# Kernel tuning notes

Hardware: AMD Instinct MI355X
Metric: run time of the kernel (lower is better)

Reference implementation:

```python
import jax, jax.numpy as jnp
import numpy as np

N = 20480    # total nodes in batched graph (64 graphs x 320 nodes)
E = 327680   # edges, avg in-degree 16
G = 64       # graphs in the batch
IN_DIM = 128
H = 4        # attention heads per layer
D = 64       # hidden dim per head (num_hidden)
C = 10       # num_classes
NEG_SLOPE = 0.2


def _gat_layer(h, src, dst, W, al, ar, residual):
    # DGL GATConv: fc -> per-head attention logits -> edge softmax over dst -> scatter-sum
    z = (h @ W).reshape(N, H, D)                       # [N,H,D]
    el = jnp.sum(z * al, axis=-1)                      # [N,H]
    er = jnp.sum(z * ar, axis=-1)                      # [N,H]
    e = jax.nn.leaky_relu(el[src] + er[dst], NEG_SLOPE)  # [E,H]
    m = jax.lax.stop_gradient(jax.ops.segment_max(e, dst, num_segments=N))
    m = jnp.where(jnp.isfinite(m), m, 0.0)
    ex = jnp.exp(e - m[dst])                           # [E,H]
    s = jax.ops.segment_sum(ex, dst, num_segments=N)   # [N,H]
    a = ex / jnp.where(s > 0, s, 1.0)[dst]             # [E,H] edge softmax
    msg = z[src] * a[:, :, None]                       # [E,H,D] (dominant intermediate)
    out = jax.ops.segment_sum(msg, dst, num_segments=N)  # [N,H,D]
    if residual:
        out = out + h.reshape(N, H, D)                 # res_fc is Identity (in == H*D)
        out = jax.nn.elu(out)                          # GATConv-internal activation
    return jax.nn.elu(out.reshape(N, H * D))           # model-level activation after flatten


def setup_inputs() -> dict:
    key = jax.random.key(0)
    ks = jax.random.split(key, 16)
    x = jax.random.normal(ks[0], (N, IN_DIM), jnp.float32)
    src = jax.random.randint(ks[1], (E,), 0, N, dtype=jnp.int32)
    # guarantee every node has >= 1 incoming edge (valid softmax denominator)
    dst = jnp.concatenate([jnp.arange(N, dtype=jnp.int32),
                           jax.random.randint(ks[2], (E - N,), 0, N, dtype=jnp.int32)])
    graph_ids = jnp.repeat(jnp.arange(G, dtype=jnp.int32), N // G)

    def lin(k, fi, fo):
        return (jax.random.normal(k, (fi, fo), jnp.float32) / np.float32(np.sqrt(fi)))

    def attn(k):
        return jax.random.normal(k, (H, D), jnp.float32) * np.float32(0.1)

    return {
        "x": x, "src": src, "dst": dst, "graph_ids": graph_ids,
        "W0": lin(ks[3], IN_DIM, H * D), "al0": attn(ks[4]), "ar0": attn(ks[5]),
        "W1": lin(ks[6], H * D, H * D), "al1": attn(ks[7]), "ar1": attn(ks[8]),
        "W2": lin(ks[9], H * D, H * D), "al2": attn(ks[10]), "ar2": attn(ks[11]),
        "Wc": lin(ks[12], H * D, C),
        "bc": jnp.zeros((C,), jnp.float32),
    }


def reference(x, src, dst, graph_ids, W0, al0, ar0, W1, al1, ar1, W2, al2, ar2, Wc, bc):
    h = _gat_layer(x, src, dst, W0, al0, ar0, residual=False)  # layer 0: no residual/act inside
    h = _gat_layer(h, src, dst, W1, al1, ar1, residual=True)
    h = _gat_layer(h, src, dst, W2, al2, ar2, residual=True)
    # dgl.mean_nodes: per-graph mean over node features
    hg = jax.ops.segment_sum(h, graph_ids, num_segments=G) / np.float32(N // G)  # [G, H*D]
    hg = jax.nn.elu(hg)
    return hg @ Wc + bc                                        # [G, C] logits
```

## Files before the change

kernel.cpp:

```cpp
#include <hip/hip_runtime.h>


#define NNODES 20480
#define NEDGES 327680
#define NGRAPH 64
#define NPG    320
#define HD     256
#define NH     4
#define NCLS   10
#define SLOTS  80

typedef __attribute__((ext_vector_type(8))) short short8;
typedef __attribute__((ext_vector_type(4))) float f32x4;

__device__ __forceinline__ float elu_f(float x)   { return x > 0.f ? x : expm1f(x); }
__device__ __forceinline__ float lrelu_f(float x) { return x > 0.f ? x : 0.2f * x; }

__device__ __forceinline__ ushort f2bf(float v) {
    uint u = __float_as_uint(v);
    uint r = (u + 0x7fffu + ((u >> 16) & 1u)) >> 16;
    return (ushort)r;
}
__device__ __forceinline__ float bf2f(ushort u) {
    return __uint_as_float(((uint)u) << 16);
}

__device__ __forceinline__ void split8(const float* __restrict__ p,
                                       short8& hi, short8& lo) {
    float4 a = *reinterpret_cast<const float4*>(p);
    float4 b = *reinterpret_cast<const float4*>(p + 4);
    float v[8] = {a.x, a.y, a.z, a.w, b.x, b.y, b.z, b.w};
    #pragma unroll
    for (int e = 0; e < 8; e++) {
        uint u = __float_as_uint(v[e]);
        hi[e] = (short)(u >> 16);
        float hf = __uint_as_float(u & 0xFFFF0000u);
        float lf = v[e] - hf;
        lo[e] = (short)(__float_as_uint(lf) >> 16);
    }
}

__global__ __launch_bounds__(256) void prep_k(
        const int* __restrict__ src, const int* __restrict__ dst,
        int* __restrict__ deg, int* __restrict__ slots,
        const float* __restrict__ W0, ushort* __restrict__ B0h, ushort* __restrict__ B0l,
        const float* __restrict__ W1, ushort* __restrict__ B1h, ushort* __restrict__ B1l,
        const float* __restrict__ W2, ushort* __restrict__ B2h, ushort* __restrict__ B2l) {
    int b = blockIdx.x;
    if (b < NEDGES / 256) {
        int e = b * 256 + threadIdx.x;
        int d = dst[e];
        int pos = atomicAdd(&deg[d], 1);
        if (pos < SLOTS) slots[d * SLOTS + pos] = src[e];
    } else {
        int idx = (b - NEDGES / 256) * 256 + threadIdx.x;
        const float* W; ushort *Bh, *Bl;
        if (idx < 128 * 256)          { W = W0; Bh = B0h; Bl = B0l; }
        else if (idx < 384 * 256)     { W = W1; Bh = B1h; Bl = B1l; idx -= 128 * 256; }
        else                          { W = W2; Bh = B2h; Bl = B2l; idx -= 384 * 256; }
        int k = idx >> 8, col = idx & 255;
        float v = W[idx];
        ushort h = f2bf(v);
        float vh = bf2f(h);
        ushort l = f2bf(v - vh);
        size_t o = (size_t)(k >> 5) * 8192 + (size_t)col * 32 + (k & 31);
        Bh[o] = h;
        Bl[o] = l;
    }
}

__global__ __launch_bounds__(256) void gemm_mfma_k(
        const float* __restrict__ A,
        const ushort* __restrict__ Bhi, const ushort* __restrict__ Blo,
        const float* __restrict__ al_, const float* __restrict__ ar_,
        ushort* __restrict__ zbf, float* __restrict__ el, float* __restrict__ er,
        int K) {
    int m0 = blockIdx.x * 32;
    int w = threadIdx.x >> 6, l = threadIdx.x & 63;
    int n0 = w * 64;
    int lr = l & 15, lk = l >> 4;
    f32x4 acc[2][4] = {};
    int ksteps = K >> 5;
    for (int kt = 0; kt < ksteps; kt++) {
        int kbase = kt * 32 + lk * 8;
        short8 a_hi[2], a_lo[2], b_hi[4], b_lo[4];
        #pragma unroll
        for (int i = 0; i < 2; i++) {
            size_t off = (size_t)(m0 + i * 16 + lr) * K + kbase;
            split8(A + off, a_hi[i], a_lo[i]);
        }
        #pragma unroll
        for (int j = 0; j < 4; j++) {
            size_t off = (size_t)kt * 8192 + (size_t)(n0 + j * 16 + lr) * 32 + lk * 8;
            b_hi[j] = *reinterpret_cast<const short8*>(Bhi + off);
            b_lo[j] = *reinterpret_cast<const short8*>(Blo + off);
        }
        #pragma unroll
        for (int i = 0; i < 2; i++)
            #pragma unroll
            for (int j = 0; j < 4; j++) {
                acc[i][j] = __builtin_amdgcn_mfma_f32_16x16x32_bf16(a_hi[i], b_hi[j], acc[i][j], 0, 0, 0);
                acc[i][j] = __builtin_amdgcn_mfma_f32_16x16x32_bf16(a_hi[i], b_lo[j], acc[i][j], 0, 0, 0);
                acc[i][j] = __builtin_amdgcn_mfma_f32_16x16x32_bf16(a_lo[i], b_hi[j], acc[i][j], 0, 0, 0);
            }
    }
    float alv[4], arv[4];
    #pragma unroll
    for (int j = 0; j < 4; j++) {
        int col = n0 + j * 16 + lr;
        alv[j] = al_[col];
        arv[j] = ar_[col];
    }
    #pragma unroll
    for (int i = 0; i < 2; i++) {
        #pragma unroll
        for (int r = 0; r < 4; r++) {
            float pel = 0.f, per = 0.f;
            #pragma unroll
            for (int j = 0; j < 4; j++) {
                float v = acc[i][j][r];
                pel += v * alv[j];
                per += v * arv[j];
                int row = m0 + i * 16 + lk * 4 + r;
                int col = n0 + j * 16 + lr;
                zbf[(size_t)row * HD + col] = f2bf(v);
            }
            #pragma unroll
            for (int off = 1; off < 16; off <<= 1) {
                pel += __shfl_xor(pel, off);
                per += __shfl_xor(per, off);
            }
            if (lr == 0) {
                int row = m0 + i * 16 + lk * 4 + r;
                el[row * NH + w] = pel;
                er[row * NH + w] = per;
            }
        }
    }
}

__global__ __launch_bounds__(256) void attn_aggr_k(
        const ushort* __restrict__ zbf,
        const float* __restrict__ el, const float* __restrict__ er,
        const int* __restrict__ deg, const int* __restrict__ slots,
        const float* __restrict__ hin, float* __restrict__ hout,
        int residual) {
    int wid = threadIdx.x >> 6, lane = threadIdx.x & 63;
    int n = blockIdx.x * 4 + wid;
    int h = lane >> 4, j16 = lane & 15;
    int hbase = lane & 48;
    int col = j16 * 4 + h * 64;
    int d = deg[n];
    if (d > SLOTS) d = SLOTS;
    const int* sl = slots + (size_t)n * SLOTS;
    float ern = er[n * NH + h];
    float4 acc = make_float4(0.f, 0.f, 0.f, 0.f);

    if (d <= 64) {
        float pv[4];
        int   sv[4];
        #pragma unroll
        for (int u = 0; u < 4; u++) {
            int k = u * 16 + j16;
            if (k < d) {
                sv[u] = sl[k];
                pv[u] = __expf(lrelu_f(el[sv[u] * NH + h] + ern));
            } else {
                sv[u] = 0;
                pv[u] = 0.f;
            }
        }
        float ssum = pv[0] + pv[1] + pv[2] + pv[3];
        #pragma unroll
        for (int off = 1; off < 16; off <<= 1) ssum += __shfl_xor(ssum, off);
        float rinv = 1.f / ssum;
        #pragma unroll
        for (int u = 0; u < 4; u++) pv[u] *= rinv;
        #pragma unroll
        for (int u = 0; u < 4; u++) {
            int kb = u * 16;
            if (kb + 16 <= d) {
                #pragma unroll
                for (int j = 0; j < 16; j++) {
                    float w = __shfl(pv[u], hbase + j);
                    int   s = __shfl(sv[u], hbase + j);
                    ushort4 zv = *reinterpret_cast<const ushort4*>(&zbf[(size_t)s * HD + col]);
                    acc.x += bf2f(zv.x) * w;
                    acc.y += bf2f(zv.y) * w;
                    acc.z += bf2f(zv.z) * w;
                    acc.w += bf2f(zv.w) * w;
                }
            } else if (kb < d) {
                int cnt = d - kb;
                for (int j = 0; j < cnt; j++) {
                    float w = __shfl(pv[u], hbase + j);
                    int   s = __shfl(sv[u], hbase + j);
                    ushort4 zv = *reinterpret_cast<const ushort4*>(&zbf[(size_t)s * HD + col]);
                    acc.x += bf2f(zv.x) * w;
                    acc.y += bf2f(zv.y) * w;
                    acc.z += bf2f(zv.z) * w;
                    acc.w += bf2f(zv.w) * w;
                }
            }
        }
    } else {
        float ssum = 0.f;
        for (int k = j16; k < d; k += 16)
            ssum += __expf(lrelu_f(el[sl[k] * NH + h] + ern));
        #pragma unroll
        for (int off = 1; off < 16; off <<= 1) ssum += __shfl_xor(ssum, off);
        float rinv = 1.f / ssum;
        for (int k = 0; k < d; k++) {
            int s = sl[k];
            float w = __expf(lrelu_f(el[s * NH + h] + ern)) * rinv;
            ushort4 zv = *reinterpret_cast<const ushort4*>(&zbf[(size_t)s * HD + col]);
            acc.x += bf2f(zv.x) * w;
            acc.y += bf2f(zv.y) * w;
            acc.z += bf2f(zv.z) * w;
            acc.w += bf2f(zv.w) * w;
        }
    }

    size_t o = (size_t)n * HD + col;
    float4 r;
    if (residual) {
        float4 hv = *reinterpret_cast<const float4*>(&hin[o]);
        r.x = elu_f(elu_f(acc.x + hv.x));
        r.y = elu_f(elu_f(acc.y + hv.y));
        r.z = elu_f(elu_f(acc.z + hv.z));
        r.w = elu_f(elu_f(acc.w + hv.w));
    } else {
        r.x = elu_f(acc.x);
        r.y = elu_f(acc.y);
        r.z = elu_f(acc.z);
        r.w = elu_f(acc.w);
    }
    *reinterpret_cast<float4*>(&hout[o]) = r;
}

__global__ __launch_bounds__(1024) void poolcls_k(const float* __restrict__ h,
                                                  const float* __restrict__ Wc,
                                                  const float* __restrict__ bc,
                                                  float* __restrict__ out) {
    __shared__ float part[4][HD];
    __shared__ float hv[HD];
    int g = blockIdx.x, t = threadIdx.x;
    int col = t & 255, q = t >> 8;
    const float* p = h + (size_t)g * NPG * HD + (size_t)q * (NPG / 4) * HD + col;
    float s = 0.f;
    for (int i = 0; i < NPG / 4; i++) s += p[(size_t)i * HD];
    part[q][col] = s;
    __syncthreads();
    if (t < HD) {
        float tot = part[0][t] + part[1][t] + part[2][t] + part[3][t];
        hv[t] = elu_f(tot * (1.0f / NPG));
    }
    __syncthreads();
    if (t < NCLS) {
        float acc = bc[t];
        for (int k = 0; k < HD; k++) acc += hv[k] * Wc[k * NCLS + t];
        out[g * NCLS + t] = acc;
    }
}

extern "C" void kernel_launch(void* const* d_in, const int* in_sizes, int n_in,
                              void* d_out, int out_size, void* d_ws, size_t ws_size,
                              hipStream_t stream) {
    const float* x   = (const float*)d_in[0];
    const int*   src = (const int*)d_in[1];
    const int*   dst = (const int*)d_in[2];
    const float* W0  = (const float*)d_in[4];
    const float* al0 = (const float*)d_in[5];
    const float* ar0 = (const float*)d_in[6];
    const float* W1  = (const float*)d_in[7];
    const float* al1 = (const float*)d_in[8];
    const float* ar1 = (const float*)d_in[9];
    const float* W2  = (const float*)d_in[10];
    const float* al2 = (const float*)d_in[11];
    const float* ar2 = (const float*)d_in[12];
    const float* Wc  = (const float*)d_in[13];
    const float* bc  = (const float*)d_in[14];
    float* out = (float*)d_out;

    char* ws = (char*)d_ws;
    size_t off = 0;
    auto alloc = [&](size_t bytes) -> void* {
        void* p = ws + off;
        off = (off + bytes + 255) & ~(size_t)255;
        return p;
    };
    float*  hbuf     = (float*)alloc((size_t)NNODES * HD * 4);
    ushort* zbf      = (ushort*)alloc((size_t)NNODES * HD * 2);
    float*  el       = (float*)alloc((size_t)NNODES * NH * 4);
    float*  er       = (float*)alloc((size_t)NNODES * NH * 4);
    int*    deg      = (int*)alloc((size_t)NNODES * 4);
    int*    slots    = (int*)alloc((size_t)NNODES * SLOTS * 4);
    ushort* B0h      = (ushort*)alloc((size_t)128 * 256 * 2);
    ushort* B0l      = (ushort*)alloc((size_t)128 * 256 * 2);
    ushort* B1h      = (ushort*)alloc((size_t)256 * 256 * 2);
    ushort* B1l      = (ushort*)alloc((size_t)256 * 256 * 2);
    ushort* B2h      = (ushort*)alloc((size_t)256 * 256 * 2);
    ushort* B2l      = (ushort*)alloc((size_t)256 * 256 * 2);

    hipMemsetAsync(deg, 0, (size_t)NNODES * 4, stream);
    prep_k<<<NEDGES / 256 + (128 + 256 + 256), 256, 0, stream>>>(
        src, dst, deg, slots,
        W0, B0h, B0l, W1, B1h, B1l, W2, B2h, B2l);

    auto layer = [&](const float* A, const ushort* Bh, const ushort* Bl,
                     const float* al_, const float* ar_,
                     const float* hin, float* hout, int K, int residual) {
        gemm_mfma_k<<<NNODES / 32, 256, 0, stream>>>(A, Bh, Bl, al_, ar_,
                                                     zbf, el, er, K);
        attn_aggr_k<<<NNODES / 4, 256, 0, stream>>>(zbf, el, er, deg, slots,
                                                    hin, hout, residual);
    };

    layer(x,    B0h, B0l, al0, ar0, nullptr, hbuf, 128, 0);
    layer(hbuf, B1h, B1l, al1, ar1, hbuf, hbuf, 256, 1);
    layer(hbuf, B2h, B2l, al2, ar2, hbuf, hbuf, 256, 1);

    poolcls_k<<<NGRAPH, 1024, 0, stream>>>(hbuf, Wc, bc, out);
}
```

Before: 280.9 us.

## Store hidden activations in bf16 and widen aggregation gathers to 16 bytes

```diff
diff --git a/kernel.cpp b/kernel.cpp
--- a/kernel.cpp
+++ b/kernel.cpp
@@ -11,6 +11,7 @@
 #define SLOTS  80
 
 typedef __attribute__((ext_vector_type(8))) short short8;
+typedef __attribute__((ext_vector_type(8))) unsigned short ushort8v;
 typedef __attribute__((ext_vector_type(4))) float f32x4;
 
 __device__ __forceinline__ float elu_f(float x)   { return x > 0.f ? x : expm1f(x); }
@@ -69,8 +70,9 @@
     }
 }
 
+template<int ABF16>
 __global__ __launch_bounds__(256) void gemm_mfma_k(
-        const float* __restrict__ A,
+        const void* __restrict__ Av,
         const ushort* __restrict__ Bhi, const ushort* __restrict__ Blo,
         const float* __restrict__ al_, const float* __restrict__ ar_,
         ushort* __restrict__ zbf, float* __restrict__ el, float* __restrict__ er,
@@ -87,7 +89,11 @@
         #pragma unroll
         for (int i = 0; i < 2; i++) {
             size_t off = (size_t)(m0 + i * 16 + lr) * K + kbase;
-            split8(A + off, a_hi[i], a_lo[i]);
+            if (ABF16) {
+                a_hi[i] = *reinterpret_cast<const short8*>((const ushort*)Av + off);
+            } else {
+                split8((const float*)Av + off, a_hi[i], a_lo[i]);
+            }
         }
         #pragma unroll
         for (int j = 0; j < 4; j++) {
@@ -101,7 +107,8 @@
             for (int j = 0; j < 4; j++) {
                 acc[i][j] = __builtin_amdgcn_mfma_f32_16x16x32_bf16(a_hi[i], b_hi[j], acc[i][j], 0, 0, 0);
                 acc[i][j] = __builtin_amdgcn_mfma_f32_16x16x32_bf16(a_hi[i], b_lo[j], acc[i][j], 0, 0, 0);
-                acc[i][j] = __builtin_amdgcn_mfma_f32_16x16x32_bf16(a_lo[i], b_hi[j], acc[i][j], 0, 0, 0);
+                if (!ABF16)
+                    acc[i][j] = __builtin_amdgcn_mfma_f32_16x16x32_bf16(a_lo[i], b_hi[j], acc[i][j], 0, 0, 0);
             }
     }
     float alv[4], arv[4];
@@ -143,18 +150,19 @@
         const ushort* __restrict__ zbf,
         const float* __restrict__ el, const float* __restrict__ er,
         const int* __restrict__ deg, const int* __restrict__ slots,
-        const float* __restrict__ hin, float* __restrict__ hout,
+        const ushort* __restrict__ hin, ushort* __restrict__ hout,
         int residual) {
     int wid = threadIdx.x >> 6, lane = threadIdx.x & 63;
     int n = blockIdx.x * 4 + wid;
     int h = lane >> 4, j16 = lane & 15;
-    int hbase = lane & 48;
-    int col = j16 * 4 + h * 64;
+    int l32 = lane & 31, half = lane >> 5;
+    int headL = l32 >> 3;
+    int col8 = l32 * 8;
     int d = deg[n];
     if (d > SLOTS) d = SLOTS;
     const int* sl = slots + (size_t)n * SLOTS;
     float ern = er[n * NH + h];
-    float4 acc = make_float4(0.f, 0.f, 0.f, 0.f);
+    float acc[8] = {};
 
     if (d <= 64) {
         float pv[4];
@@ -178,31 +186,22 @@
         for (int u = 0; u < 4; u++) pv[u] *= rinv;
         #pragma unroll
         for (int u = 0; u < 4; u++) {
-            int kb = u * 16;
-            if (kb + 16 <= d) {
-                #pragma unroll
-                for (int j = 0; j < 16; j++) {
-                    float w = __shfl(pv[u], hbase + j);
-                    int   s = __shfl(sv[u], hbase + j);
-                    ushort4 zv = *reinterpret_cast<const ushort4*>(&zbf[(size_t)s * HD + col]);
-                    acc.x += bf2f(zv.x) * w;
-                    acc.y += bf2f(zv.y) * w;
-                    acc.z += bf2f(zv.z) * w;
-                    acc.w += bf2f(zv.w) * w;
+            if (u * 16 >= d) break;
+            #pragma unroll
+            for (int jj = 0; jj < 8; jj++) {
+                int e = u * 16 + jj * 2 + half;
+                int srcl = headL * 16 + jj * 2 + half;
+                float w = __shfl(pv[u], srcl);
+                int   s = __shfl(sv[u], srcl);
+                if (e < d) {
+                    ushort8v zv = *reinterpret_cast<const ushort8v*>(&zbf[(size_t)s * HD + col8]);
+                    #pragma unroll
+                    for (int t = 0; t < 8; t++) acc[t] += bf2f(zv[t]) * w;
                 }
-            } else if (kb < d) {
-                int cnt = d - kb;
-                for (int j = 0; j < cnt; j++) {
-                    float w = __shfl(pv[u], hbase + j);
-                    int   s = __shfl(sv[u], hbase + j);
-                    ushort4 zv = *reinterpret_cast<const ushort4*>(&zbf[(size_t)s * HD + col]);
-                    acc.x += bf2f(zv.x) * w;
-                    acc.y += bf2f(zv.y) * w;
-                    acc.z += bf2f(zv.z) * w;
-                    acc.w += bf2f(zv.w) * w;
-                }
-            }
-        }
+            }
+        }
+        #pragma unroll
+        for (int t = 0; t < 8; t++) acc[t] += __shfl_xor(acc[t], 32);
     } else {
         float ssum = 0.f;
         for (int k = j16; k < d; k += 16)
@@ -210,35 +209,35 @@
         #pragma unroll
         for (int off = 1; off < 16; off <<= 1) ssum += __shfl_xor(ssum, off);
         float rinv = 1.f / ssum;
+        float rinvL = __shfl(rinv, headL * 16);
+        float ernL = er[n * NH + headL];
         for (int k = 0; k < d; k++) {
             int s = sl[k];
-            float w = __expf(lrelu_f(el[s * NH + h] + ern)) * rinv;
-            ushort4 zv = *reinterpret_cast<const ushort4*>(&zbf[(size_t)s * HD + col]);
-            acc.x += bf2f(zv.x) * w;
-            acc.y += bf2f(zv.y) * w;
-            acc.z += bf2f(zv.z) * w;
-            acc.w += bf2f(zv.w) * w;
-        }
-    }
-
-    size_t o = (size_t)n * HD + col;
-    float4 r;
-    if (residual) {
-        float4 hv = *reinterpret_cast<const float4*>(&hin[o]);
-        r.x = elu_f(elu_f(acc.x + hv.x));
-        r.y = elu_f(elu_f(acc.y + hv.y));
-        r.z = elu_f(elu_f(acc.z + hv.z));
-        r.w = elu_f(elu_f(acc.w + hv.w));
-    } else {
-        r.x = elu_f(acc.x);
-        r.y = elu_f(acc.y);
-        r.z = elu_f(acc.z);
-        r.w = elu_f(acc.w);
-    }
-    *reinterpret_cast<float4*>(&hout[o]) = r;
-}
-
-__global__ __launch_bounds__(1024) void poolcls_k(const float* __restrict__ h,
+            float w = __expf(lrelu_f(el[s * NH + headL] + ernL)) * rinvL;
+            ushort8v zv = *reinterpret_cast<const ushort8v*>(&zbf[(size_t)s * HD + col8]);
+            #pragma unroll
+            for (int t = 0; t < 8; t++) acc[t] += bf2f(zv[t]) * w;
+        }
+    }
+
+    if (half == 0) {
+        size_t o = (size_t)n * HD + col8;
+        ushort8v r;
+        if (residual) {
+            ushort8v hv = *reinterpret_cast<const ushort8v*>(&hin[o]);
+            #pragma unroll
+            for (int t = 0; t < 8; t++)
+                r[t] = f2bf(elu_f(elu_f(acc[t] + bf2f(hv[t]))));
+        } else {
+            #pragma unroll
+            for (int t = 0; t < 8; t++)
+                r[t] = f2bf(elu_f(acc[t]));
+        }
+        *reinterpret_cast<ushort8v*>(&hout[o]) = r;
+    }
+}
+
+__global__ __launch_bounds__(1024) void poolcls_k(const ushort* __restrict__ h,
                                                   const float* __restrict__ Wc,
                                                   const float* __restrict__ bc,
                                                   float* __restrict__ out) {
@@ -246,9 +245,9 @@
     __shared__ float hv[HD];
     int g = blockIdx.x, t = threadIdx.x;
     int col = t & 255, q = t >> 8;
-    const float* p = h + (size_t)g * NPG * HD + (size_t)q * (NPG / 4) * HD + col;
+    const ushort* p = h + (size_t)g * NPG * HD + (size_t)q * (NPG / 4) * HD + col;
     float s = 0.f;
-    for (int i = 0; i < NPG / 4; i++) s += p[(size_t)i * HD];
+    for (int i = 0; i < NPG / 4; i++) s += bf2f(p[(size_t)i * HD]);
     part[q][col] = s;
     __syncthreads();
     if (t < HD) {
@@ -289,7 +288,7 @@
         off = (off + bytes + 255) & ~(size_t)255;
         return p;
     };
-    float*  hbuf     = (float*)alloc((size_t)NNODES * HD * 4);
+    ushort* hbuf     = (ushort*)alloc((size_t)NNODES * HD * 2);
     ushort* zbf      = (ushort*)alloc((size_t)NNODES * HD * 2);
     float*  el       = (float*)alloc((size_t)NNODES * NH * 4);
     float*  er       = (float*)alloc((size_t)NNODES * NH * 4);
@@ -307,18 +306,18 @@
         src, dst, deg, slots,
         W0, B0h, B0l, W1, B1h, B1l, W2, B2h, B2l);
 
-    auto layer = [&](const float* A, const ushort* Bh, const ushort* Bl,
-                     const float* al_, const float* ar_,
-                     const float* hin, float* hout, int K, int residual) {
-        gemm_mfma_k<<<NNODES / 32, 256, 0, stream>>>(A, Bh, Bl, al_, ar_,
-                                                     zbf, el, er, K);
-        attn_aggr_k<<<NNODES / 4, 256, 0, stream>>>(zbf, el, er, deg, slots,
-                                                    hin, hout, residual);
-    };
-
-    layer(x,    B0h, B0l, al0, ar0, nullptr, hbuf, 128, 0);
-    layer(hbuf, B1h, B1l, al1, ar1, hbuf, hbuf, 256, 1);
-    layer(hbuf, B2h, B2l, al2, ar2, hbuf, hbuf, 256, 1);
+    gemm_mfma_k<0><<<NNODES / 32, 256, 0, stream>>>(x, B0h, B0l, al0, ar0,
+                                                    zbf, el, er, 128);
+    attn_aggr_k<<<NNODES / 4, 256, 0, stream>>>(zbf, el, er, deg, slots,
+                                                nullptr, hbuf, 0);
+    gemm_mfma_k<1><<<NNODES / 32, 256, 0, stream>>>(hbuf, B1h, B1l, al1, ar1,
+                                                    zbf, el, er, 256);
+    attn_aggr_k<<<NNODES / 4, 256, 0, stream>>>(zbf, el, er, deg, slots,
+                                                hbuf, hbuf, 1);
+    gemm_mfma_k<1><<<NNODES / 32, 256, 0, stream>>>(hbuf, B2h, B2l, al2, ar2,
+                                                    zbf, el, er, 256);
+    attn_aggr_k<<<NNODES / 4, 256, 0, stream>>>(zbf, el, er, deg, slots,
+                                                hbuf, hbuf, 1);
 
     poolcls_k<<<NGRAPH, 1024, 0, stream>>>(hbuf, Wc, bc, out);
 }
```

After: 275.4 us. -2.0%, faster.
